# Performance work log

Hardware: AMD Instinct MI355X
Metric: run time of the kernel (lower is better)

The kernel has to match this reference:

```python
import jax, jax.numpy as jnp
import numpy as np

B, N, D, H, P = 16, 1024, 768, 12, 16
HD = D // H
FF = 4 * D
SCALE = HD ** -0.5


def _layer_norm(x, g, b, eps=1e-5):
    mu = jnp.mean(x, axis=-1, keepdims=True)
    var = jnp.var(x, axis=-1, keepdims=True)
    return (x - mu) * jax.lax.rsqrt(var + eps) * g + b


def setup_inputs() -> dict:
    key = jax.random.key(0)
    ks = jax.random.split(key, 8)
    s = 0.02
    return {
        "x": jax.random.normal(ks[0], (B, N, D), jnp.float32),
        "prompt": jax.random.normal(ks[1], (B, 2, P, H, HD), jnp.float32),
        "qkv_w": jax.random.normal(ks[2], (3 * D, D), jnp.float32) * s,
        "qkv_b": jnp.zeros((3 * D,), jnp.float32),
        "out_w": jax.random.normal(ks[3], (D, D), jnp.float32) * s,
        "out_b": jnp.zeros((D,), jnp.float32),
        "ln1_g": jnp.ones((D,), jnp.float32),
        "ln1_b": jnp.zeros((D,), jnp.float32),
        "ln2_g": jnp.ones((D,), jnp.float32),
        "ln2_b": jnp.zeros((D,), jnp.float32),
        "fc1_w": jax.random.normal(ks[4], (FF, D), jnp.float32) * s,
        "fc1_b": jnp.zeros((FF,), jnp.float32),
        "fc2_w": jax.random.normal(ks[5], (D, FF), jnp.float32) * s,
        "fc2_b": jnp.zeros((D,), jnp.float32),
    }


def reference(x, prompt, qkv_w, qkv_b, out_w, out_b, ln1_g, ln1_b,
              ln2_g, ln2_b, fc1_w, fc1_b, fc2_w, fc2_b):
    # --- attention branch ---
    h = _layer_norm(x, ln1_g, ln1_b)                       # [B,N,D]
    qkv = h @ qkv_w.T + qkv_b                              # [B,N,3D]
    qkv = qkv.reshape(B, N, 3, H, HD).transpose(2, 0, 3, 1, 4)  # [3,B,H,N,hd]
    q, k, v = qkv[0], qkv[1], qkv[2]
    # prompt [B,2,P,H,hd] -> [2,B,H,P,hd]
    pr = jnp.transpose(prompt, (1, 0, 3, 2, 4))
    k = jnp.concatenate([pr[0], k], axis=2)                # [B,H,P+N,hd]
    v = jnp.concatenate([pr[1], v], axis=2)
    attn = jnp.einsum("bhqd,bhkd->bhqk", q, k) * SCALE     # [B,H,N,P+N]
    attn = jax.nn.softmax(attn, axis=-1)
    o = jnp.einsum("bhqk,bhkd->bhqd", attn, v)             # [B,H,N,hd]
    o = o.transpose(0, 2, 1, 3).reshape(B, N, D)
    o = o @ out_w.T + out_b
    x = x + o
    # --- MLP branch (CLIP: c_fc -> QuickGELU -> c_proj) ---
    h2 = _layer_norm(x, ln2_g, ln2_b)
    m = h2 @ fc1_w.T + fc1_b
    m = m * jax.nn.sigmoid(1.702 * m)                      # QuickGELU
    m = m @ fc2_w.T + fc2_b
    return x + m
```

## Files before the change

kernel.cpp:

```cpp
#include <hip/hip_runtime.h>
#include <hip/hip_bf16.h>

typedef __bf16 bf16;
typedef __attribute__((ext_vector_type(8))) __bf16 bf16x8;
typedef __attribute__((ext_vector_type(4))) __bf16 bf16x4;
typedef __attribute__((ext_vector_type(4))) short s16x4;
typedef __attribute__((ext_vector_type(4))) float f32x4;

#define GLOBAL_AS __attribute__((address_space(1)))
#define LDS_AS __attribute__((address_space(3)))

constexpr int B_  = 16;
constexpr int N_  = 1024;
constexpr int D_  = 768;
constexpr int H_  = 12;
constexpr int P_  = 16;
constexpr int FF_ = 3072;
constexpr int BN_ = B_ * N_;
constexpr int LP_ = 1088;
constexpr float EXPC_ = 0.18033688f;

__global__ __launch_bounds__(256) void cvt_kernel(
    const float* __restrict__ s0, const float* __restrict__ s1,
    const float* __restrict__ s2, const float* __restrict__ s3,
    bf16* __restrict__ d0, bf16* __restrict__ d1,
    bf16* __restrict__ d2, bf16* __restrict__ d3)
{
    int i = (blockIdx.x * 256 + threadIdx.x) * 4;
    const float* s; bf16* d; int off;
    if (i < 1769472)      { s = s0; d = d0; off = i; }
    else if (i < 2359296) { s = s1; d = d1; off = i - 1769472; }
    else if (i < 4718592) { s = s2; d = d2; off = i - 2359296; }
    else                  { s = s3; d = d3; off = i - 4718592; }
    float4 f = *(const float4*)(s + off);
    bf16x4 o;
    o[0] = (bf16)f.x; o[1] = (bf16)f.y; o[2] = (bf16)f.z; o[3] = (bf16)f.w;
    *(bf16x4*)(d + off) = o;
}

__global__ __launch_bounds__(256) void prep_kernel(
    const float* __restrict__ prompt, bf16* __restrict__ Kall,
    bf16* __restrict__ VTall)
{
    int hb = blockIdx.x;
    int b = hb / 12, h = hb % 12;
    int t = threadIdx.x;
    size_t kbase = (size_t)hb * LP_ * 64;
    size_t vbase = (size_t)hb * 64 * LP_;

    {
        int p = t >> 4, d0 = (t & 15) * 4;
        const float* src = prompt + (((size_t)(b * 2 + 0) * P_ + p) * H_ + h) * 64 + d0;
        float4 f = *(const float4*)src;
        bf16x4 o4;
        o4[0] = (bf16)f.x; o4[1] = (bf16)f.y; o4[2] = (bf16)f.z; o4[3] = (bf16)f.w;
        *(bf16x4*)(Kall + kbase + (size_t)p * 64 + d0) = o4;
    }
    {
        int d = t >> 2, p0 = (t & 3) * 4;
        bf16x4 o4;
#pragma unroll
        for (int j = 0; j < 4; j++)
            o4[j] = (bf16)prompt[(((size_t)(b * 2 + 1) * P_ + p0 + j) * H_ + h) * 64 + d];
        *(bf16x4*)(VTall + vbase + (size_t)d * LP_ + p0) = o4;
    }
    {
        bf16* kp = Kall + kbase + 1040 * 64 + (size_t)t * 12;
#pragma unroll
        for (int i = 0; i < 12; i++) kp[i] = (bf16)0.f;
        int d = t >> 2, j0 = (t & 3) * 12;
        bf16* vp = VTall + vbase + (size_t)d * LP_ + 1040 + j0;
#pragma unroll
        for (int i = 0; i < 12; i++) vp[i] = (bf16)0.f;
    }
}

template <typename T>
__global__ __launch_bounds__(256) void ln_kernel(
    const T* __restrict__ x, const float* __restrict__ g,
    const float* __restrict__ bta, bf16* __restrict__ out)
{
    int row = blockIdx.x;
    const T* xr = x + (size_t)row * D_;
    int t = threadIdx.x;
    float v[3];
    float s = 0.f, ss = 0.f;
#pragma unroll
    for (int i = 0; i < 3; i++) {
        v[i] = (float)xr[t + i * 256];
        s += v[i];
        ss += v[i] * v[i];
    }
#pragma unroll
    for (int o = 32; o > 0; o >>= 1) {
        s  += __shfl_down(s, o);
        ss += __shfl_down(ss, o);
    }
    __shared__ float red_s[4], red_ss[4];
    int w = t >> 6, lane = t & 63;
    if (lane == 0) { red_s[w] = s; red_ss[w] = ss; }
    __syncthreads();
    s  = red_s[0] + red_s[1] + red_s[2] + red_s[3];
    ss = red_ss[0] + red_ss[1] + red_ss[2] + red_ss[3];
    float mu = s * (1.f / 768.f);
    float var = ss * (1.f / 768.f) - mu * mu;
    float rstd = rsqrtf(var + 1e-5f);
#pragma unroll
    for (int i = 0; i < 3; i++) {
        int c = t + i * 256;
        out[(size_t)row * D_ + c] = (bf16)((v[i] - mu) * rstd * g[c] + bta[c]);
    }
}

template <int EPI>
__global__ __launch_bounds__(256, 4) void gemm_bt(
    const bf16* __restrict__ A, const bf16* __restrict__ Bt,
    const float* __restrict__ bias,
    const float* __restrict__ resF, const bf16* __restrict__ resB,
    float* __restrict__ outF, bf16* __restrict__ outB,
    bf16* __restrict__ Qall, bf16* __restrict__ Kall, bf16* __restrict__ VTall,
    int M, int N, int K)
{
    __shared__ bf16 As[128 * 64];
    __shared__ bf16 Bs[128 * 64];

    const int nb = gridDim.x;
    const int gx = N >> 7;
    const int bid = blockIdx.x;
    const int tile = (bid & 7) * (nb >> 3) + (bid >> 3);
    const int rowBase = (tile / gx) * 128;
    const int colBase = (tile % gx) * 128;

    const int tid = threadIdx.x;
    const int w = tid >> 6, lane = tid & 63;
    const int wr = w >> 1, wc = w & 1;
    const int lrow = lane & 15, khalf = lane >> 4;

    f32x4 acc[4][4];
#pragma unroll
    for (int mi = 0; mi < 4; mi++)
#pragma unroll
        for (int ni = 0; ni < 4; ni++)
            acc[mi][ni] = (f32x4){0.f, 0.f, 0.f, 0.f};

    for (int k0 = 0; k0 < K; k0 += 64) {
#pragma unroll
        for (int i = 0; i < 4; i++) {
            int idx = i * 256 + w * 64 + lane;
            int r = idx >> 3, c = idx & 7;
            int cs = c ^ (r & 7);
            __builtin_amdgcn_global_load_lds(
                (const GLOBAL_AS void*)(A + (size_t)(rowBase + r) * K + k0 + cs * 8),
                (LDS_AS void*)(As + (size_t)idx * 8), 16, 0, 0);
        }
#pragma unroll
        for (int i = 0; i < 4; i++) {
            int idx = i * 256 + w * 64 + lane;
            int r = idx >> 3, c = idx & 7;
            int cs = c ^ (r & 7);
            __builtin_amdgcn_global_load_lds(
                (const GLOBAL_AS void*)(Bt + (size_t)(colBase + r) * K + k0 + cs * 8),
                (LDS_AS void*)(Bs + (size_t)idx * 8), 16, 0, 0);
        }
        __syncthreads();

#pragma unroll
        for (int ks = 0; ks < 2; ks++) {
            bf16x8 af[4], bfr[4];
#pragma unroll
            for (int mi = 0; mi < 4; mi++) {
                int rr = wr * 64 + mi * 16 + lrow;
                int ch = (ks * 4 + khalf) ^ (rr & 7);
                af[mi] = *(const bf16x8*)(As + (size_t)rr * 64 + ch * 8);
            }
#pragma unroll
            for (int ni = 0; ni < 4; ni++) {
                int rr = wc * 64 + ni * 16 + lrow;
                int ch = (ks * 4 + khalf) ^ (rr & 7);
                bfr[ni] = *(const bf16x8*)(Bs + (size_t)rr * 64 + ch * 8);
            }
#pragma unroll
            for (int mi = 0; mi < 4; mi++)
#pragma unroll
                for (int ni = 0; ni < 4; ni++)
                    acc[mi][ni] = __builtin_amdgcn_mfma_f32_16x16x32_bf16(
                        af[mi], bfr[ni], acc[mi][ni], 0, 0, 0);
        }
        __syncthreads();
    }

#pragma unroll
    for (int mi = 0; mi < 4; mi++) {
#pragma unroll
        for (int ni = 0; ni < 4; ni++) {
            int col = colBase + wc * 64 + ni * 16 + lrow;
            int row0 = rowBase + wr * 64 + mi * 16 + khalf * 4;
            float bv = bias[col];
            if constexpr (EPI == 3) {
                int sect = (col >= 1536) ? 2 : (col >= 768 ? 1 : 0);
                int hh = (col >> 6) - sect * 12;
                int dd = col & 63;
                int bb = row0 >> 10, n0 = row0 & 1023;
                size_t bh = (size_t)bb * 12 + hh;
                if (sect == 0) {
                    bf16* qp = Qall + (bh * 1024 + n0) * 64 + dd;
#pragma unroll
                    for (int r = 0; r < 4; r++)
                        qp[(size_t)r * 64] = (bf16)((acc[mi][ni][r] + bv) * EXPC_);
                } else if (sect == 1) {
                    bf16* kp = Kall + bh * (LP_ * 64) + (size_t)(16 + n0) * 64 + dd;
#pragma unroll
                    for (int r = 0; r < 4; r++)
                        kp[(size_t)r * 64] = (bf16)(acc[mi][ni][r] + bv);
                } else {
                    bf16x4 pv;
#pragma unroll
                    for (int r = 0; r < 4; r++)
                        pv[r] = (bf16)(acc[mi][ni][r] + bv);
                    *(bf16x4*)(VTall + bh * (64 * LP_) + (size_t)dd * LP_ + 16 + n0) = pv;
                }
            } else {
#pragma unroll
                for (int r = 0; r < 4; r++) {
                    size_t idx = (size_t)(row0 + r) * N + col;
                    float v = acc[mi][ni][r] + bv;
                    if constexpr (EPI == 1) {
                        outF[idx] = v + (float)resB[idx];
                    } else if constexpr (EPI == 2) {
                        outB[idx] = (bf16)(v / (1.f + __expf(-1.702f * v)));
                    } else {
                        outB[idx] = (bf16)(v + resF[idx]);
                    }
                }
            }
        }
    }
}

__global__ __launch_bounds__(256, 3) void attn_kernel(
    const bf16* __restrict__ Qall, const bf16* __restrict__ Kall,
    const bf16* __restrict__ VTall, bf16* __restrict__ o)
{
    __shared__ bf16 Ks[2][64 * 72];
    __shared__ bf16 Vt[2][64 * 72];

    const int lid = blockIdx.x;
    const int xcd = lid & 7, slot = lid >> 3;
    const int hb = xcd * 24 + (slot >> 3);
    const int qt = slot & 7;
    const int h = hb % 12, b = hb / 12;

    const int tid = threadIdx.x;
    const int w = tid >> 6, lane = tid & 63;
    const int lrow = lane & 15, q4 = lane >> 4;

    bf16x8 qf[2][2];
    {
        const bf16* qb = Qall + ((size_t)hb * 1024 + qt * 128 + w * 32 + lrow) * 64 + q4 * 8;
        qf[0][0] = *(const bf16x8*)(qb);
        qf[0][1] = *(const bf16x8*)(qb + 32);
        qf[1][0] = *(const bf16x8*)(qb + 16 * 64);
        qf[1][1] = *(const bf16x8*)(qb + 16 * 64 + 32);
    }

    f32x4 acc_o[4][2];
#pragma unroll
    for (int dj = 0; dj < 4; dj++)
#pragma unroll
        for (int mi = 0; mi < 2; mi++)
            acc_o[dj][mi] = (f32x4){0.f, 0.f, 0.f, 0.f};
    float lp[2] = {0.f, 0.f};

    const bf16* kg = Kall + (size_t)hb * LP_ * 64;
    const bf16* vg = VTall + (size_t)hb * 64 * LP_;
    const int r_ = tid >> 2;
    const int c_ = (tid & 3) * 16;

    bf16x8 k0 = *(const bf16x8*)(kg + (size_t)r_ * 64 + c_);
    bf16x8 k1 = *(const bf16x8*)(kg + (size_t)r_ * 64 + c_ + 8);
    bf16x8 v0 = *(const bf16x8*)(vg + (size_t)r_ * LP_ + c_);
    bf16x8 v1 = *(const bf16x8*)(vg + (size_t)r_ * LP_ + c_ + 8);

    for (int kt = 0; kt < 17; kt++) {
        bf16* ksb = &Ks[kt & 1][0];
        bf16* vtb = &Vt[kt & 1][0];
        *(bf16x8*)(ksb + r_ * 72 + c_)     = k0;
        *(bf16x8*)(ksb + r_ * 72 + c_ + 8) = k1;
        *(bf16x8*)(vtb + r_ * 72 + c_)     = v0;
        *(bf16x8*)(vtb + r_ * 72 + c_ + 8) = v1;
        __syncthreads();

        int nkt = (kt < 16) ? kt + 1 : 16;
        k0 = *(const bf16x8*)(kg + (size_t)nkt * 4096 + (size_t)r_ * 64 + c_);
        k1 = *(const bf16x8*)(kg + (size_t)nkt * 4096 + (size_t)r_ * 64 + c_ + 8);
        v0 = *(const bf16x8*)(vg + (size_t)r_ * LP_ + nkt * 64 + c_);
        v1 = *(const bf16x8*)(vg + (size_t)r_ * LP_ + nkt * 64 + c_ + 8);

        f32x4 st[4][2];
#pragma unroll
        for (int kb = 0; kb < 4; kb++)
#pragma unroll
            for (int mi = 0; mi < 2; mi++)
                st[kb][mi] = (f32x4){0.f, 0.f, 0.f, 0.f};
#pragma unroll
        for (int kb = 0; kb < 4; kb++) {
#pragma unroll
            for (int ks = 0; ks < 2; ks++) {
                bf16x8 kf = *(const bf16x8*)(ksb + (size_t)(kb * 16 + lrow) * 72 +
                                             ks * 32 + q4 * 8);
                st[kb][0] = __builtin_amdgcn_mfma_f32_16x16x32_bf16(kf, qf[0][ks], st[kb][0], 0, 0, 0);
                st[kb][1] = __builtin_amdgcn_mfma_f32_16x16x32_bf16(kf, qf[1][ks], st[kb][1], 0, 0, 0);
            }
        }

        s16x4 pfrag[4][2];
#pragma unroll
        for (int kb = 0; kb < 4; kb++) {
#pragma unroll
            for (int mi = 0; mi < 2; mi++) {
                float e0 = __builtin_amdgcn_exp2f(st[kb][mi][0]);
                float e1 = __builtin_amdgcn_exp2f(st[kb][mi][1]);
                float e2 = __builtin_amdgcn_exp2f(st[kb][mi][2]);
                float e3 = __builtin_amdgcn_exp2f(st[kb][mi][3]);
                if (kt < 16 || kb == 0)
                    lp[mi] += (e0 + e1) + (e2 + e3);
                bf16x4 pb;
                pb[0] = (bf16)e0; pb[1] = (bf16)e1; pb[2] = (bf16)e2; pb[3] = (bf16)e3;
                pfrag[kb][mi] = __builtin_bit_cast(s16x4, pb);
            }
        }

#pragma unroll
        for (int dj = 0; dj < 4; dj++) {
#pragma unroll
            for (int kb = 0; kb < 4; kb++) {
                bf16x4 vf = *(const bf16x4*)(vtb + (size_t)(dj * 16 + lrow) * 72 +
                                             kb * 16 + q4 * 4);
                s16x4 vfs = __builtin_bit_cast(s16x4, vf);
                acc_o[dj][0] = __builtin_amdgcn_mfma_f32_16x16x16bf16_1k(
                    vfs, pfrag[kb][0], acc_o[dj][0], 0, 0, 0);
                acc_o[dj][1] = __builtin_amdgcn_mfma_f32_16x16x16bf16_1k(
                    vfs, pfrag[kb][1], acc_o[dj][1], 0, 0, 0);
            }
        }
    }

    float linv[2];
#pragma unroll
    for (int mi = 0; mi < 2; mi++) {
        float ls = lp[mi];
        ls += __shfl_xor(ls, 16);
        ls += __shfl_xor(ls, 32);
        linv[mi] = 1.f / ls;
    }

    bf16* ob = o + (size_t)(b * N_ + qt * 128 + w * 32) * 768 + h * 64;
#pragma unroll
    for (int mi = 0; mi < 2; mi++) {
#pragma unroll
        for (int dj = 0; dj < 4; dj++) {
            bf16x4 ov;
#pragma unroll
            for (int r = 0; r < 4; r++)
                ov[r] = (bf16)(acc_o[dj][mi][r] * linv[mi]);
            *(bf16x4*)(ob + (size_t)(mi * 16 + lrow) * 768 + dj * 16 + q4 * 4) = ov;
        }
    }
}

extern "C" void kernel_launch(void* const* d_in, const int* in_sizes, int n_in,
                              void* d_out, int out_size, void* d_ws, size_t ws_size,
                              hipStream_t stream)
{
    const float* x      = (const float*)d_in[0];
    const float* prompt = (const float*)d_in[1];
    const float* qkv_w  = (const float*)d_in[2];
    const float* qkv_b  = (const float*)d_in[3];
    const float* out_w  = (const float*)d_in[4];
    const float* out_b  = (const float*)d_in[5];
    const float* ln1_g  = (const float*)d_in[6];
    const float* ln1_b  = (const float*)d_in[7];
    const float* ln2_g  = (const float*)d_in[8];
    const float* ln2_b  = (const float*)d_in[9];
    const float* fc1_w  = (const float*)d_in[10];
    const float* fc1_b  = (const float*)d_in[11];
    const float* fc2_w  = (const float*)d_in[12];
    const float* fc2_b  = (const float*)d_in[13];
    float* out = (float*)d_out;

    bf16* qkvw_b = (bf16*)d_ws;
    bf16* outw_b = qkvw_b + 1769472;
    bf16* fc1w_b = outw_b + 589824;
    bf16* fc2w_b = fc1w_b + 2359296;
    bf16* h_b    = fc2w_b + 2359296;
    bf16* o_b    = h_b    + 12582912;
    bf16* Qall   = o_b    + 12582912;
    bf16* Kall   = Qall   + 12582912;
    bf16* VTall  = Kall   + 13369344;
    bf16* mid    = o_b;
    bf16* x1b    = VTall + 13369344;

    cvt_kernel<<<6912, 256, 0, stream>>>(qkv_w, out_w, fc1_w, fc2_w,
                                         qkvw_b, outw_b, fc1w_b, fc2w_b);
    prep_kernel<<<192, 256, 0, stream>>>(prompt, Kall, VTall);
    ln_kernel<float><<<BN_, 256, 0, stream>>>(x, ln1_g, ln1_b, h_b);
    gemm_bt<3><<<18 * 128, 256, 0, stream>>>(h_b, qkvw_b, qkv_b, nullptr, nullptr,
                                             nullptr, nullptr, Qall, Kall, VTall,
                                             BN_, 2304, 768);
    attn_kernel<<<1536, 256, 0, stream>>>(Qall, Kall, VTall, o_b);
    gemm_bt<4><<<6 * 128, 256, 0, stream>>>(o_b, outw_b, out_b, x, nullptr,
                                            nullptr, x1b, nullptr, nullptr, nullptr,
                                            BN_, 768, 768);
    ln_kernel<bf16><<<BN_, 256, 0, stream>>>(x1b, ln2_g, ln2_b, h_b);
    gemm_bt<2><<<24 * 128, 256, 0, stream>>>(h_b, fc1w_b, fc1_b, nullptr, nullptr,
                                             nullptr, mid, nullptr, nullptr, nullptr,
                                             BN_, FF_, 768);
    gemm_bt<1><<<6 * 128, 256, 0, stream>>>(mid, fc2w_b, fc2_b, nullptr, x1b,
                                            out, nullptr, nullptr, nullptr, nullptr,
                                            BN_, 768, FF_);
}
```

Before: 503.4 us.

## Double-buffer GEMM LDS tiles with register prefetch; merge cvt and prep kernels

The GEMM main loop changes from direct global-to-LDS loads of 64-wide K tiles with two barriers per step to 32-wide K tiles. These go through a register prefetch into double-buffered LDS with a single barrier per step, so the next tile's global loads overlap the current MFMAs. The LDS swizzle is redone for the 32-element row layout. Separately, the weight conversion and prompt prep kernels are merged into one launch to save a kernel dispatch. The smaller K step halves MFMA work per barrier and loses the global_load_lds path, which may offset the overlap gain.

```diff
diff --git a/kernel.cpp b/kernel.cpp
--- a/kernel.cpp
+++ b/kernel.cpp
@@ -20,41 +20,39 @@
 constexpr int LP_ = 1088;
 constexpr float EXPC_ = 0.18033688f;
 
-__global__ __launch_bounds__(256) void cvt_kernel(
+__global__ __launch_bounds__(256) void cvt_prep_kernel(
     const float* __restrict__ s0, const float* __restrict__ s1,
     const float* __restrict__ s2, const float* __restrict__ s3,
     bf16* __restrict__ d0, bf16* __restrict__ d1,
-    bf16* __restrict__ d2, bf16* __restrict__ d3)
-{
-    int i = (blockIdx.x * 256 + threadIdx.x) * 4;
-    const float* s; bf16* d; int off;
-    if (i < 1769472)      { s = s0; d = d0; off = i; }
-    else if (i < 2359296) { s = s1; d = d1; off = i - 1769472; }
-    else if (i < 4718592) { s = s2; d = d2; off = i - 2359296; }
-    else                  { s = s3; d = d3; off = i - 4718592; }
-    float4 f = *(const float4*)(s + off);
-    bf16x4 o;
-    o[0] = (bf16)f.x; o[1] = (bf16)f.y; o[2] = (bf16)f.z; o[3] = (bf16)f.w;
-    *(bf16x4*)(d + off) = o;
-}
-
-__global__ __launch_bounds__(256) void prep_kernel(
+    bf16* __restrict__ d2, bf16* __restrict__ d3,
     const float* __restrict__ prompt, bf16* __restrict__ Kall,
     bf16* __restrict__ VTall)
 {
-    int hb = blockIdx.x;
+    int t = threadIdx.x;
+    if (blockIdx.x < 6912) {
+        int i = (blockIdx.x * 256 + t) * 4;
+        const float* s; bf16* d; int off;
+        if (i < 1769472)      { s = s0; d = d0; off = i; }
+        else if (i < 2359296) { s = s1; d = d1; off = i - 1769472; }
+        else if (i < 4718592) { s = s2; d = d2; off = i - 2359296; }
+        else                  { s = s3; d = d3; off = i - 4718592; }
+        float4 f = *(const float4*)(s + off);
+        bf16x4 o;
+        o[0] = (bf16)f.x; o[1] = (bf16)f.y; o[2] = (bf16)f.z; o[3] = (bf16)f.w;
+        *(bf16x4*)(d + off) = o;
+        return;
+    }
+    int hb = blockIdx.x - 6912;
     int b = hb / 12, h = hb % 12;
-    int t = threadIdx.x;
     size_t kbase = (size_t)hb * LP_ * 64;
     size_t vbase = (size_t)hb * 64 * LP_;
-
     {
-        int p = t >> 4, d0 = (t & 15) * 4;
-        const float* src = prompt + (((size_t)(b * 2 + 0) * P_ + p) * H_ + h) * 64 + d0;
+        int p = t >> 4, d0i = (t & 15) * 4;
+        const float* src = prompt + (((size_t)(b * 2 + 0) * P_ + p) * H_ + h) * 64 + d0i;
         float4 f = *(const float4*)src;
         bf16x4 o4;
         o4[0] = (bf16)f.x; o4[1] = (bf16)f.y; o4[2] = (bf16)f.z; o4[3] = (bf16)f.w;
-        *(bf16x4*)(Kall + kbase + (size_t)p * 64 + d0) = o4;
+        *(bf16x4*)(Kall + kbase + (size_t)p * 64 + d0i) = o4;
     }
     {
         int d = t >> 2, p0 = (t & 3) * 4;
@@ -121,8 +119,8 @@
     bf16* __restrict__ Qall, bf16* __restrict__ Kall, bf16* __restrict__ VTall,
     int M, int N, int K)
 {
-    __shared__ bf16 As[128 * 64];
-    __shared__ bf16 Bs[128 * 64];
+    __shared__ bf16 As[2][128 * 32];
+    __shared__ bf16 Bs[2][128 * 32];
 
     const int nb = gridDim.x;
     const int gx = N >> 7;
@@ -136,6 +134,15 @@
     const int wr = w >> 1, wc = w & 1;
     const int lrow = lane & 15, khalf = lane >> 4;
 
+    const int sr = tid >> 1;
+    const int c0 = (tid & 1) * 2;
+    const int ssw = (sr >> 1) & 3;
+    const int pL0 = sr * 32 + ((c0 ^ ssw) * 8);
+    const int pL1 = sr * 32 + (((c0 + 1) ^ ssw) * 8);
+
+    const bf16* ag = A + (size_t)(rowBase + sr) * K + c0 * 8;
+    const bf16* bg = Bt + (size_t)(colBase + sr) * K + c0 * 8;
+
     f32x4 acc[4][4];
 #pragma unroll
     for (int mi = 0; mi < 4; mi++)
@@ -143,50 +150,42 @@
         for (int ni = 0; ni < 4; ni++)
             acc[mi][ni] = (f32x4){0.f, 0.f, 0.f, 0.f};
 
-    for (int k0 = 0; k0 < K; k0 += 64) {
-#pragma unroll
-        for (int i = 0; i < 4; i++) {
-            int idx = i * 256 + w * 64 + lane;
-            int r = idx >> 3, c = idx & 7;
-            int cs = c ^ (r & 7);
-            __builtin_amdgcn_global_load_lds(
-                (const GLOBAL_AS void*)(A + (size_t)(rowBase + r) * K + k0 + cs * 8),
-                (LDS_AS void*)(As + (size_t)idx * 8), 16, 0, 0);
-        }
-#pragma unroll
-        for (int i = 0; i < 4; i++) {
-            int idx = i * 256 + w * 64 + lane;
-            int r = idx >> 3, c = idx & 7;
-            int cs = c ^ (r & 7);
-            __builtin_amdgcn_global_load_lds(
-                (const GLOBAL_AS void*)(Bt + (size_t)(colBase + r) * K + k0 + cs * 8),
-                (LDS_AS void*)(Bs + (size_t)idx * 8), 16, 0, 0);
-        }
+    bf16x8 pa0 = *(const bf16x8*)(ag);
+    bf16x8 pa1 = *(const bf16x8*)(ag + 8);
+    bf16x8 pb0 = *(const bf16x8*)(bg);
+    bf16x8 pb1 = *(const bf16x8*)(bg + 8);
+
+#pragma unroll 2
+    for (int k0 = 0; k0 < K; k0 += 32) {
+        const int buf = (k0 >> 5) & 1;
+        *(bf16x8*)(&As[buf][pL0]) = pa0;
+        *(bf16x8*)(&As[buf][pL1]) = pa1;
+        *(bf16x8*)(&Bs[buf][pL0]) = pb0;
+        *(bf16x8*)(&Bs[buf][pL1]) = pb1;
+        int kn = (k0 + 32 < K) ? (k0 + 32) : k0;
+        pa0 = *(const bf16x8*)(ag + kn);
+        pa1 = *(const bf16x8*)(ag + kn + 8);
+        pb0 = *(const bf16x8*)(bg + kn);
+        pb1 = *(const bf16x8*)(bg + kn + 8);
         __syncthreads();
 
-#pragma unroll
-        for (int ks = 0; ks < 2; ks++) {
-            bf16x8 af[4], bfr[4];
-#pragma unroll
-            for (int mi = 0; mi < 4; mi++) {
-                int rr = wr * 64 + mi * 16 + lrow;
-                int ch = (ks * 4 + khalf) ^ (rr & 7);
-                af[mi] = *(const bf16x8*)(As + (size_t)rr * 64 + ch * 8);
-            }
-#pragma unroll
-            for (int ni = 0; ni < 4; ni++) {
-                int rr = wc * 64 + ni * 16 + lrow;
-                int ch = (ks * 4 + khalf) ^ (rr & 7);
-                bfr[ni] = *(const bf16x8*)(Bs + (size_t)rr * 64 + ch * 8);
-            }
-#pragma unroll
-            for (int mi = 0; mi < 4; mi++)
-#pragma unroll
-                for (int ni = 0; ni < 4; ni++)
-                    acc[mi][ni] = __builtin_amdgcn_mfma_f32_16x16x32_bf16(
-                        af[mi], bfr[ni], acc[mi][ni], 0, 0, 0);
-        }
-        __syncthreads();
+        bf16x8 af[4], bfr[4];
+#pragma unroll
+        for (int mi = 0; mi < 4; mi++) {
+            int rr = wr * 64 + mi * 16 + lrow;
+            af[mi] = *(const bf16x8*)(&As[buf][rr * 32 + ((khalf ^ ((rr >> 1) & 3)) * 8)]);
+        }
+#pragma unroll
+        for (int ni = 0; ni < 4; ni++) {
+            int rr = wc * 64 + ni * 16 + lrow;
+            bfr[ni] = *(const bf16x8*)(&Bs[buf][rr * 32 + ((khalf ^ ((rr >> 1) & 3)) * 8)]);
+        }
+#pragma unroll
+        for (int mi = 0; mi < 4; mi++)
+#pragma unroll
+            for (int ni = 0; ni < 4; ni++)
+                acc[mi][ni] = __builtin_amdgcn_mfma_f32_16x16x32_bf16(
+                    af[mi], bfr[ni], acc[mi][ni], 0, 0, 0);
     }
 
 #pragma unroll
@@ -400,9 +399,9 @@
     bf16* mid    = o_b;
     bf16* x1b    = VTall + 13369344;
 
-    cvt_kernel<<<6912, 256, 0, stream>>>(qkv_w, out_w, fc1_w, fc2_w,
-                                         qkvw_b, outw_b, fc1w_b, fc2w_b);
-    prep_kernel<<<192, 256, 0, stream>>>(prompt, Kall, VTall);
+    cvt_prep_kernel<<<7104, 256, 0, stream>>>(qkv_w, out_w, fc1_w, fc2_w,
+                                              qkvw_b, outw_b, fc1w_b, fc2w_b,
+                                              prompt, Kall, VTall);
     ln_kernel<float><<<BN_, 256, 0, stream>>>(x, ln1_g, ln1_b, h_b);
     gemm_bt<3><<<18 * 128, 256, 0, stream>>>(h_b, qkvw_b, qkv_b, nullptr, nullptr,
                                              nullptr, nullptr, Qall, Kall, VTall,
```

After: 589.0 us. 1.17x slower.
